# Optimization experiments

Hardware: AMD Instinct MI355X
Metric: run time of the kernel (lower is better)

## Reference

```python
import jax, jax.numpy as jnp
import numpy as np

N = 100000
E = 3200000
F_IN = 128
HID = 64
NUM_GRAPHS = 512
NUM_CLASSES = 2


def setup_inputs() -> dict:
    key = jax.random.key(0)
    ks = jax.random.split(key, 8)
    x = jax.random.normal(ks[0], (N, F_IN), dtype=jnp.float32)
    edge_index = jax.random.randint(ks[1], (2, E), 0, N, dtype=jnp.int64)
    batch = jnp.sort(jax.random.randint(ks[2], (N,), 0, NUM_GRAPHS, dtype=jnp.int64))
    # Glorot-style init for GCN weights, PyTorch default-style for fc
    W1 = jax.random.normal(ks[3], (F_IN, HID), dtype=jnp.float32) * (1.0 / np.sqrt(F_IN))
    b1 = jnp.zeros((HID,), dtype=jnp.float32)
    W2 = jax.random.normal(ks[4], (HID, HID), dtype=jnp.float32) * (1.0 / np.sqrt(HID))
    b2 = jnp.zeros((HID,), dtype=jnp.float32)
    Wfc = jax.random.normal(ks[5], (HID, NUM_CLASSES), dtype=jnp.float32) * (1.0 / np.sqrt(HID))
    bfc = jax.random.normal(ks[6], (NUM_CLASSES,), dtype=jnp.float32) * 0.01
    return {"x": x, "edge_index": edge_index, "batch": batch,
            "W1": W1, "b1": b1, "W2": W2, "b2": b2, "Wfc": Wfc, "bfc": bfc}


def _gcn_conv(x, row, col, deg_inv_sqrt, W, b):
    """PyG GCNConv: out[col] += d^{-1/2}[row] d^{-1/2}[col] * (x W)[row], self-loops included in row/col."""
    h = x @ W  # [N, out_dim]
    norm = deg_inv_sqrt[row] * deg_inv_sqrt[col]  # [E+N]
    msgs = h[row] * norm[:, None]  # gather + scale
    out = jax.ops.segment_sum(msgs, col, num_segments=N)  # scatter-add
    return out + b


def reference(x, edge_index, batch, W1, b1, W2, b2, Wfc, bfc):
    # add self-loops once (shared normalization for both layers)
    loop = jnp.arange(N, dtype=edge_index.dtype)
    row = jnp.concatenate([edge_index[0], loop])  # sources
    col = jnp.concatenate([edge_index[1], loop])  # targets
    deg = jax.ops.segment_sum(jnp.ones_like(col, dtype=x.dtype), col, num_segments=N)
    deg_inv_sqrt = jnp.where(deg > 0, jax.lax.rsqrt(deg), 0.0)

    h = jax.nn.relu(_gcn_conv(x, row, col, deg_inv_sqrt, W1, b1))
    h = jax.nn.relu(_gcn_conv(h, row, col, deg_inv_sqrt, W2, b2))

    # global_mean_pool over batch ids
    sums = jax.ops.segment_sum(h, batch, num_segments=NUM_GRAPHS)  # [G, HID]
    counts = jax.ops.segment_sum(jnp.ones((N,), dtype=h.dtype), batch, num_segments=NUM_GRAPHS)
    pooled = sums / jnp.maximum(counts, 1.0)[:, None]

    # dropout p=0.5 is identity in eval mode
    return pooled @ Wfc + bfc  # [G, NUM_CLASSES]
```

## Files before the change

### kernel.cpp

```cpp
#include <hip/hip_runtime.h>

#define N_NODES   100000
#define N_EDGES   3200000
#define F_INP     128
#define HID       64
#define N_GRAPHS  512
#define N_CLASSES 2
#define BSH       8
#define BSZ       256
#define NB        391
#define SCAT_BLOCKS 1024
#define CHUNK     (N_EDGES / SCAT_BLOCKS)
#define CAP2      8960

__device__ __forceinline__ unsigned short f2bf(float f) {
    unsigned int u = __float_as_uint(f);
    return (unsigned short)((u + 0x7FFFu + ((u >> 16) & 1u)) >> 16);
}
__device__ __forceinline__ float bf_lo(unsigned int u) { return __uint_as_float(u << 16); }
__device__ __forceinline__ float bf_hi(unsigned int u) { return __uint_as_float(u & 0xFFFF0000u); }

__global__ __launch_bounds__(256) void scatterX(const int* __restrict__ ei,
                                                int* __restrict__ gcur,
                                                int* __restrict__ pairs) {
    __shared__ int lcnt[NB];
    __shared__ int lbase[NB];
    __shared__ int lcur[NB];
    const int tid = threadIdx.x;
    for (int i = tid; i < NB; i += 256) { lcnt[i] = 0; lcur[i] = 0; }
    __syncthreads();
    const int e0 = blockIdx.x * CHUNK;
    for (int e = e0 + tid; e < e0 + CHUNK; e += 256)
        atomicAdd(&lcnt[ei[N_EDGES + e] >> BSH], 1);
    __syncthreads();
    for (int i = tid; i < NB; i += 256) {
        int c = lcnt[i];
        lbase[i] = c ? atomicAdd(&gcur[i], c) : 0;
    }
    __syncthreads();
    for (int e = e0 + tid; e < e0 + CHUNK; e += 256) {
        int c = ei[N_EDGES + e];
        int r = ei[e];
        int b = c >> BSH;
        int off = atomicAdd(&lcur[b], 1);
        int pos = lbase[b] + off;
        if (pos < CAP2)
            pairs[b * CAP2 + pos] = r | ((c & (BSZ - 1)) << 17);
    }
}

__global__ __launch_bounds__(512) void bscan_kernel(const int* __restrict__ gcur,
                                                    int* __restrict__ boff,
                                                    int* __restrict__ offs) {
    __shared__ int s[512];
    const int tid = threadIdx.x;
    const int v = (tid < NB) ? min(gcur[tid], CAP2) : 0;
    s[tid] = v;
    __syncthreads();
    for (int d = 1; d < 512; d <<= 1) {
        int t = (tid >= d) ? s[tid - d] : 0;
        __syncthreads();
        s[tid] += t;
        __syncthreads();
    }
    if (tid <= NB) boff[tid] = s[tid] - v;
    if (tid == NB) offs[N_NODES] = s[tid];
}

__global__ __launch_bounds__(512) void csrX(const int* __restrict__ pairs,
                                            const int* __restrict__ gcur,
                                            const int* __restrict__ boff,
                                            int* __restrict__ adj,
                                            int* __restrict__ offs,
                                            float* __restrict__ dis) {
    __shared__ int sedge[CAP2];
    __shared__ int cnt[BSZ];
    __shared__ int sc[BSZ];
    __shared__ int base[BSZ];
    __shared__ int cur[BSZ];
    const int tid = threadIdx.x;
    const int b = blockIdx.x;
    const int m = min(gcur[b], CAP2);
    const int dst = boff[b];
    if (tid < BSZ) { cnt[tid] = 0; cur[tid] = 0; }
    __syncthreads();
    for (int i = tid; i < m; i += 512) {
        int v = pairs[b * CAP2 + i];
        sedge[i] = v;
        atomicAdd(&cnt[v >> 17], 1);
    }
    __syncthreads();
    if (tid < BSZ) sc[tid] = cnt[tid];
    __syncthreads();
    for (int d = 1; d < BSZ; d <<= 1) {
        int t = (tid >= d && tid < BSZ) ? sc[tid - d] : 0;
        __syncthreads();
        if (tid < BSZ) sc[tid] += t;
        __syncthreads();
    }
    if (tid < BSZ) base[tid] = dst + sc[tid] - cnt[tid];
    __syncthreads();
    for (int i = tid; i < m; i += 512) {
        int v = sedge[i];
        int lc = v >> 17;
        int o = atomicAdd(&cur[lc], 1);
        adj[base[lc] + o] = v & 131071;
    }
    const int n = (b << BSH) + tid;
    if (tid < BSZ && n < N_NODES) {
        offs[n] = base[tid];
        dis[n] = rsqrtf((float)cnt[tid] + 1.0f);
    }
}

#define MM1_ROWS 32
#define XS_LD    132
__global__ __launch_bounds__(256) void mm1_kernel(const float* __restrict__ x,
                                                  const float* __restrict__ W1,
                                                  const float* __restrict__ dis,
                                                  unsigned short* __restrict__ p) {
    __shared__ float xs[MM1_ROWS * XS_LD];
    __shared__ float ws[F_INP * HID];
    for (int i = threadIdx.x; i < F_INP * HID / 4; i += 256)
        ((float4*)ws)[i] = ((const float4*)W1)[i];
    const int row_base = blockIdx.x * MM1_ROWS;
    for (int i = threadIdx.x; i < MM1_ROWS * (F_INP / 4); i += 256) {
        int r = i >> 5, c4 = i & 31;
        int gr = row_base + r;
        float4 v = make_float4(0.f, 0.f, 0.f, 0.f);
        if (gr < N_NODES) v = *(const float4*)(x + (size_t)gr * F_INP + c4 * 4);
        *(float4*)(xs + r * XS_LD + c4 * 4) = v;
    }
    __syncthreads();
    const int tx = threadIdx.x & 15;
    const int ty = threadIdx.x >> 4;
    float acc[2][4] = {};
#pragma unroll 4
    for (int k = 0; k < F_INP; k += 4) {
        float4 a0 = *(const float4*)(xs + ty * XS_LD + k);
        float4 a1 = *(const float4*)(xs + (ty + 16) * XS_LD + k);
        float4 w0 = *(const float4*)(ws + (k + 0) * HID + tx * 4);
        float4 w1 = *(const float4*)(ws + (k + 1) * HID + tx * 4);
        float4 w2 = *(const float4*)(ws + (k + 2) * HID + tx * 4);
        float4 w3 = *(const float4*)(ws + (k + 3) * HID + tx * 4);
        acc[0][0] += a0.x * w0.x + a0.y * w1.x + a0.z * w2.x + a0.w * w3.x;
        acc[0][1] += a0.x * w0.y + a0.y * w1.y + a0.z * w2.y + a0.w * w3.y;
        acc[0][2] += a0.x * w0.z + a0.y * w1.z + a0.z * w2.z + a0.w * w3.z;
        acc[0][3] += a0.x * w0.w + a0.y * w1.w + a0.z * w2.w + a0.w * w3.w;
        acc[1][0] += a1.x * w0.x + a1.y * w1.x + a1.z * w2.x + a1.w * w3.x;
        acc[1][1] += a1.x * w0.y + a1.y * w1.y + a1.z * w2.y + a1.w * w3.y;
        acc[1][2] += a1.x * w0.z + a1.y * w1.z + a1.z * w2.z + a1.w * w3.z;
        acc[1][3] += a1.x * w0.w + a1.y * w1.w + a1.z * w2.w + a1.w * w3.w;
    }
#pragma unroll
    for (int i = 0; i < 2; ++i) {
        int rr = row_base + ty + 16 * i;
        if (rr < N_NODES) {
            float d = dis[rr];
            ushort4 o;
            o.x = f2bf(d * acc[i][0]);
            o.y = f2bf(d * acc[i][1]);
            o.z = f2bf(d * acc[i][2]);
            o.w = f2bf(d * acc[i][3]);
            *(ushort4*)(p + (size_t)rr * HID + tx * 4) = o;
        }
    }
}

#define HS_LD 72
__global__ __launch_bounds__(256) void mm2_kernel(const unsigned short* __restrict__ hb,
                                                  const float* __restrict__ W2,
                                                  const float* __restrict__ dis,
                                                  unsigned short* __restrict__ p) {
    __shared__ unsigned short hs[64 * HS_LD];
    __shared__ float ws[HID * HID];
    for (int i = threadIdx.x; i < HID * HID / 4; i += 256)
        ((float4*)ws)[i] = ((const float4*)W2)[i];
    const int row_base = blockIdx.x * 64;
    for (int i = threadIdx.x; i < 64 * (HID / 8); i += 256) {
        int r = i >> 3, c8 = i & 7;
        int gr = row_base + r;
        uint4 v = make_uint4(0u, 0u, 0u, 0u);
        if (gr < N_NODES) v = *(const uint4*)(hb + (size_t)gr * HID + c8 * 8);
        *(uint4*)(hs + r * HS_LD + c8 * 8) = v;
    }
    __syncthreads();
    const int tx = threadIdx.x & 15;
    const int ty = threadIdx.x >> 4;
    float acc[4][4] = {};
#pragma unroll 2
    for (int k = 0; k < HID; k += 8) {
        uint4 a[4];
#pragma unroll
        for (int i = 0; i < 4; ++i)
            a[i] = *(const uint4*)(hs + (ty + 16 * i) * HS_LD + k);
        float4 w[8];
#pragma unroll
        for (int m = 0; m < 8; ++m)
            w[m] = *(const float4*)(ws + (k + m) * HID + tx * 4);
#pragma unroll
        for (int i = 0; i < 4; ++i) {
            float h0 = bf_lo(a[i].x), h1 = bf_hi(a[i].x);
            float h2 = bf_lo(a[i].y), h3 = bf_hi(a[i].y);
            float h4 = bf_lo(a[i].z), h5 = bf_hi(a[i].z);
            float h6 = bf_lo(a[i].w), h7 = bf_hi(a[i].w);
            acc[i][0] += h0 * w[0].x + h1 * w[1].x + h2 * w[2].x + h3 * w[3].x
                       + h4 * w[4].x + h5 * w[5].x + h6 * w[6].x + h7 * w[7].x;
            acc[i][1] += h0 * w[0].y + h1 * w[1].y + h2 * w[2].y + h3 * w[3].y
                       + h4 * w[4].y + h5 * w[5].y + h6 * w[6].y + h7 * w[7].y;
            acc[i][2] += h0 * w[0].z + h1 * w[1].z + h2 * w[2].z + h3 * w[3].z
                       + h4 * w[4].z + h5 * w[5].z + h6 * w[6].z + h7 * w[7].z;
            acc[i][3] += h0 * w[0].w + h1 * w[1].w + h2 * w[2].w + h3 * w[3].w
                       + h4 * w[4].w + h5 * w[5].w + h6 * w[6].w + h7 * w[7].w;
        }
    }
#pragma unroll
    for (int i = 0; i < 4; ++i) {
        int rr = row_base + ty + 16 * i;
        if (rr < N_NODES) {
            float d = dis[rr];
            ushort4 o;
            o.x = f2bf(d * acc[i][0]);
            o.y = f2bf(d * acc[i][1]);
            o.z = f2bf(d * acc[i][2]);
            o.w = f2bf(d * acc[i][3]);
            *(ushort4*)(p + (size_t)rr * HID + tx * 4) = o;
        }
    }
}

__device__ __forceinline__ float gather_node(const unsigned short* __restrict__ p,
                                             const int* __restrict__ adj,
                                             int c, int beg, int end, int q, int g) {
    float acc[8];
    {
        uint4 s = *(const uint4*)(p + (size_t)c * HID + g * 8);
        float sm = (q == 0) ? 1.f : 0.f;
        acc[0] = sm * bf_lo(s.x); acc[1] = sm * bf_hi(s.x);
        acc[2] = sm * bf_lo(s.y); acc[3] = sm * bf_hi(s.y);
        acc[4] = sm * bf_lo(s.z); acc[5] = sm * bf_hi(s.z);
        acc[6] = sm * bf_lo(s.w); acc[7] = sm * bf_hi(s.w);
    }
    int e = beg;
    for (; e + 32 <= end; e += 32) {
        int r0 = adj[e + q];
        int r1 = adj[e + 8 + q];
        int r2 = adj[e + 16 + q];
        int r3 = adj[e + 24 + q];
        uint4 v0 = *(const uint4*)(p + (size_t)r0 * HID + g * 8);
        uint4 v1 = *(const uint4*)(p + (size_t)r1 * HID + g * 8);
        uint4 v2 = *(const uint4*)(p + (size_t)r2 * HID + g * 8);
        uint4 v3 = *(const uint4*)(p + (size_t)r3 * HID + g * 8);
        acc[0] += (bf_lo(v0.x) + bf_lo(v1.x)) + (bf_lo(v2.x) + bf_lo(v3.x));
        acc[1] += (bf_hi(v0.x) + bf_hi(v1.x)) + (bf_hi(v2.x) + bf_hi(v3.x));
        acc[2] += (bf_lo(v0.y) + bf_lo(v1.y)) + (bf_lo(v2.y) + bf_lo(v3.y));
        acc[3] += (bf_hi(v0.y) + bf_hi(v1.y)) + (bf_hi(v2.y) + bf_hi(v3.y));
        acc[4] += (bf_lo(v0.z) + bf_lo(v1.z)) + (bf_lo(v2.z) + bf_lo(v3.z));
        acc[5] += (bf_hi(v0.z) + bf_hi(v1.z)) + (bf_hi(v2.z) + bf_hi(v3.z));
        acc[6] += (bf_lo(v0.w) + bf_lo(v1.w)) + (bf_lo(v2.w) + bf_lo(v3.w));
        acc[7] += (bf_hi(v0.w) + bf_hi(v1.w)) + (bf_hi(v2.w) + bf_hi(v3.w));
    }
    for (; e + 16 <= end; e += 16) {
        int r0 = adj[e + q];
        int r1 = adj[e + 8 + q];
        uint4 v0 = *(const uint4*)(p + (size_t)r0 * HID + g * 8);
        uint4 v1 = *(const uint4*)(p + (size_t)r1 * HID + g * 8);
        acc[0] += bf_lo(v0.x) + bf_lo(v1.x); acc[1] += bf_hi(v0.x) + bf_hi(v1.x);
        acc[2] += bf_lo(v0.y) + bf_lo(v1.y); acc[3] += bf_hi(v0.y) + bf_hi(v1.y);
        acc[4] += bf_lo(v0.z) + bf_lo(v1.z); acc[5] += bf_hi(v0.z) + bf_hi(v1.z);
        acc[6] += bf_lo(v0.w) + bf_lo(v1.w); acc[7] += bf_hi(v0.w) + bf_hi(v1.w);
    }
    for (; e < end; e += 8) {
        int idx = e + q;
        int r = adj[min(idx, end - 1)];
        float m = (idx < end) ? 1.f : 0.f;
        uint4 v = *(const uint4*)(p + (size_t)r * HID + g * 8);
        acc[0] = fmaf(m, bf_lo(v.x), acc[0]); acc[1] = fmaf(m, bf_hi(v.x), acc[1]);
        acc[2] = fmaf(m, bf_lo(v.y), acc[2]); acc[3] = fmaf(m, bf_hi(v.y), acc[3]);
        acc[4] = fmaf(m, bf_lo(v.z), acc[4]); acc[5] = fmaf(m, bf_hi(v.z), acc[5]);
        acc[6] = fmaf(m, bf_lo(v.w), acc[6]); acc[7] = fmaf(m, bf_hi(v.w), acc[7]);
    }
    const bool q0 = (q & 1) != 0, q1 = (q & 2) != 0, q2 = (q & 4) != 0;
    float b0 = (q0 ? acc[1] : acc[0]) + __shfl_xor(q0 ? acc[0] : acc[1], 8, 64);
    float b1 = (q0 ? acc[3] : acc[2]) + __shfl_xor(q0 ? acc[2] : acc[3], 8, 64);
    float b2 = (q0 ? acc[5] : acc[4]) + __shfl_xor(q0 ? acc[4] : acc[5], 8, 64);
    float b3 = (q0 ? acc[7] : acc[6]) + __shfl_xor(q0 ? acc[6] : acc[7], 8, 64);
    float c0 = (q1 ? b1 : b0) + __shfl_xor(q1 ? b0 : b1, 16, 64);
    float c1 = (q1 ? b3 : b2) + __shfl_xor(q1 ? b2 : b3, 16, 64);
    return (q2 ? c1 : c0) + __shfl_xor(q2 ? c0 : c1, 32, 64);
}

__global__ __launch_bounds__(256) void gather1_kernel(const unsigned short* __restrict__ p,
                                                      const int* __restrict__ adj,
                                                      const int* __restrict__ offs,
                                                      const float* __restrict__ dis,
                                                      const float* __restrict__ b1,
                                                      unsigned short* __restrict__ hb) {
    const int lane = threadIdx.x & 63;
    const int q = lane >> 3, g = lane & 7;
    const int gwave = (blockIdx.x * blockDim.x + threadIdx.x) >> 6;
    const int nwaves = (gridDim.x * blockDim.x) >> 6;
    const int per = (N_NODES + nwaves - 1) / nwaves;
    const int c0 = gwave * per;
    const int c1 = min(N_NODES, c0 + per);
    const float bj = b1[g * 8 + q];
    if (c0 >= c1) return;
    int beg = offs[c0];
    for (int c = c0; c < c1; ++c) {
        const int end = offs[c + 1];
        float val = gather_node(p, adj, c, beg, end, q, g);
        hb[(size_t)c * HID + g * 8 + q] = f2bf(fmaxf(dis[c] * val + bj, 0.f));
        beg = end;
    }
}

__global__ __launch_bounds__(256) void gather2_kernel(const unsigned short* __restrict__ p,
                                                      const int* __restrict__ adj,
                                                      const int* __restrict__ offs,
                                                      const float* __restrict__ dis,
                                                      const float* __restrict__ b2,
                                                      const int* __restrict__ batch,
                                                      float* __restrict__ sums) {
    const int lane = threadIdx.x & 63;
    const int q = lane >> 3, g = lane & 7;
    const int gwave = (blockIdx.x * blockDim.x + threadIdx.x) >> 6;
    const int nwaves = (gridDim.x * blockDim.x) >> 6;
    const int per = (N_NODES + nwaves - 1) / nwaves;
    const int c0 = gwave * per;
    const int c1 = min(N_NODES, c0 + per);
    const float bj = b2[g * 8 + q];
    const int feat = g * 8 + q;
    float part = 0.f;
    int gc = -1;
    if (c0 >= c1) return;
    int beg = offs[c0];
    for (int c = c0; c < c1; ++c) {
        const int end = offs[c + 1];
        float val = gather_node(p, adj, c, beg, end, q, g);
        float v = fmaxf(dis[c] * val + bj, 0.f);
        int gid = batch[c];
        if (gid != gc) {
            if (gc >= 0) atomicAdd(&sums[(size_t)gc * HID + feat], part);
            part = 0.f;
            gc = gid;
        }
        part += v;
        beg = end;
    }
    if (gc >= 0) atomicAdd(&sums[(size_t)gc * HID + feat], part);
}

__global__ void fc_kernel(const float* __restrict__ sums, const int* __restrict__ batch,
                          const float* __restrict__ Wfc, const float* __restrict__ bfc,
                          float* __restrict__ out) {
    const int g = blockIdx.x;
    const int j = threadIdx.x;
    int lo = 0, hi = N_NODES;
    while (lo < hi) { int m = (lo + hi) >> 1; if (batch[m] < g) lo = m + 1; else hi = m; }
    const int l0 = lo;
    lo = 0; hi = N_NODES;
    while (lo < hi) { int m = (lo + hi) >> 1; if (batch[m] < g + 1) lo = m + 1; else hi = m; }
    float cnt = fmaxf((float)(lo - l0), 1.0f);
    float pj = sums[(size_t)g * HID + j] / cnt;
    float a0 = pj * Wfc[j * N_CLASSES + 0];
    float a1 = pj * Wfc[j * N_CLASSES + 1];
    for (int off = 32; off > 0; off >>= 1) {
        a0 += __shfl_down(a0, off, 64);
        a1 += __shfl_down(a1, off, 64);
    }
    if (j == 0) {
        out[g * N_CLASSES + 0] = a0 + bfc[0];
        out[g * N_CLASSES + 1] = a1 + bfc[1];
    }
}

extern "C" void kernel_launch(void* const* d_in, const int* in_sizes, int n_in,
                              void* d_out, int out_size, void* d_ws, size_t ws_size,
                              hipStream_t stream) {
    const float* x     = (const float*)d_in[0];
    const int*   ei    = (const int*)d_in[1];
    const int*   batch = (const int*)d_in[2];
    const float* W1    = (const float*)d_in[3];
    const float* b1    = (const float*)d_in[4];
    const float* W2    = (const float*)d_in[5];
    const float* b2    = (const float*)d_in[6];
    const float* Wfc   = (const float*)d_in[7];
    const float* bfc   = (const float*)d_in[8];
    float* out = (float*)d_out;

    char* ws = (char*)d_ws;
    size_t off = 0;
    auto alloc = [&](size_t bytes) -> void* {
        void* pp = ws + off;
        off += (bytes + 255) & ~(size_t)255;
        return pp;
    };
    int*   gcur   = (int*)alloc((size_t)NB * 4);
    float* sums   = (float*)alloc((size_t)N_GRAPHS * HID * 4);
    int*   boff   = (int*)alloc((size_t)(NB + 1) * 4);
    int*   offs   = (int*)alloc((size_t)(N_NODES + 1) * 4);
    float* dis    = (float*)alloc((size_t)N_NODES * 4);
    int*   pairs  = (int*)alloc((size_t)NB * CAP2 * 4);
    int*   adj    = (int*)alloc((size_t)N_EDGES * 4);
    unsigned short* p  = (unsigned short*)alloc((size_t)N_NODES * HID * 2);
    unsigned short* hb = (unsigned short*)alloc((size_t)N_NODES * HID * 2);

    hipMemsetAsync(gcur, 0, (size_t)((char*)(sums + N_GRAPHS * HID) - (char*)gcur), stream);

    scatterX<<<SCAT_BLOCKS, 256, 0, stream>>>(ei, gcur, pairs);
    bscan_kernel<<<1, 512, 0, stream>>>(gcur, boff, offs);
    csrX<<<NB, 512, 0, stream>>>(pairs, gcur, boff, adj, offs, dis);
    mm1_kernel<<<(N_NODES + MM1_ROWS - 1) / MM1_ROWS, 256, 0, stream>>>(x, W1, dis, p);
    gather1_kernel<<<2048, 256, 0, stream>>>(p, adj, offs, dis, b1, hb);
    mm2_kernel<<<(N_NODES + 63) / 64, 256, 0, stream>>>(hb, W2, dis, p);
    gather2_kernel<<<2048, 256, 0, stream>>>(p, adj, offs, dis, b2, batch, sums);
    fc_kernel<<<N_GRAPHS, 64, 0, stream>>>(sums, batch, Wfc, bfc, out);
}
```

Before: 363.3 us.

## Fuse edge scatter with first matmul and fold block scan into CSR build

Measured after the change: 348.2 us. -4.2%, faster.

```diff
diff --git a/kernel.cpp b/kernel.cpp
--- a/kernel.cpp
+++ b/kernel.cpp
@@ -9,9 +9,12 @@
 #define BSH       8
 #define BSZ       256
 #define NB        391
-#define SCAT_BLOCKS 1024
+#define SCAT_BLOCKS 256
 #define CHUNK     (N_EDGES / SCAT_BLOCKS)
 #define CAP2      8960
+#define MM1_ROWS  32
+#define XS_LD     132
+#define MM1_BLOCKS ((N_NODES + MM1_ROWS - 1) / MM1_ROWS)
 
 __device__ __forceinline__ unsigned short f2bf(float f) {
     unsigned int u = __float_as_uint(f);
@@ -20,68 +23,109 @@
 __device__ __forceinline__ float bf_lo(unsigned int u) { return __uint_as_float(u << 16); }
 __device__ __forceinline__ float bf_hi(unsigned int u) { return __uint_as_float(u & 0xFFFF0000u); }
 
-__global__ __launch_bounds__(256) void scatterX(const int* __restrict__ ei,
-                                                int* __restrict__ gcur,
-                                                int* __restrict__ pairs) {
-    __shared__ int lcnt[NB];
-    __shared__ int lbase[NB];
-    __shared__ int lcur[NB];
+__global__ __launch_bounds__(256) void fused_pre(const int* __restrict__ ei,
+                                                 int* __restrict__ gcur,
+                                                 int* __restrict__ pairs,
+                                                 const float* __restrict__ x,
+                                                 const float* __restrict__ W1,
+                                                 float* __restrict__ praw) {
+    __shared__ __align__(16) char smem[(MM1_ROWS * XS_LD + F_INP * HID) * 4];
     const int tid = threadIdx.x;
-    for (int i = tid; i < NB; i += 256) { lcnt[i] = 0; lcur[i] = 0; }
-    __syncthreads();
-    const int e0 = blockIdx.x * CHUNK;
-    for (int e = e0 + tid; e < e0 + CHUNK; e += 256)
-        atomicAdd(&lcnt[ei[N_EDGES + e] >> BSH], 1);
-    __syncthreads();
-    for (int i = tid; i < NB; i += 256) {
-        int c = lcnt[i];
-        lbase[i] = c ? atomicAdd(&gcur[i], c) : 0;
-    }
-    __syncthreads();
-    for (int e = e0 + tid; e < e0 + CHUNK; e += 256) {
-        int c = ei[N_EDGES + e];
-        int r = ei[e];
-        int b = c >> BSH;
-        int off = atomicAdd(&lcur[b], 1);
-        int pos = lbase[b] + off;
-        if (pos < CAP2)
-            pairs[b * CAP2 + pos] = r | ((c & (BSZ - 1)) << 17);
-    }
-}
-
-__global__ __launch_bounds__(512) void bscan_kernel(const int* __restrict__ gcur,
-                                                    int* __restrict__ boff,
-                                                    int* __restrict__ offs) {
-    __shared__ int s[512];
-    const int tid = threadIdx.x;
-    const int v = (tid < NB) ? min(gcur[tid], CAP2) : 0;
-    s[tid] = v;
-    __syncthreads();
-    for (int d = 1; d < 512; d <<= 1) {
-        int t = (tid >= d) ? s[tid - d] : 0;
-        __syncthreads();
-        s[tid] += t;
-        __syncthreads();
-    }
-    if (tid <= NB) boff[tid] = s[tid] - v;
-    if (tid == NB) offs[N_NODES] = s[tid];
+    if (blockIdx.x < SCAT_BLOCKS) {
+        int* lcnt = (int*)smem;
+        int* lbase = lcnt + NB;
+        int* lcur = lbase + NB;
+        for (int i = tid; i < NB; i += 256) { lcnt[i] = 0; lcur[i] = 0; }
+        __syncthreads();
+        const int e0 = blockIdx.x * CHUNK;
+        for (int e = e0 + tid; e < e0 + CHUNK; e += 256)
+            atomicAdd(&lcnt[ei[N_EDGES + e] >> BSH], 1);
+        __syncthreads();
+        for (int i = tid; i < NB; i += 256) {
+            int c = lcnt[i];
+            lbase[i] = c ? atomicAdd(&gcur[i], c) : 0;
+        }
+        __syncthreads();
+        for (int e = e0 + tid; e < e0 + CHUNK; e += 256) {
+            int c = ei[N_EDGES + e];
+            int r = ei[e];
+            int b = c >> BSH;
+            int off = atomicAdd(&lcur[b], 1);
+            int pos = lbase[b] + off;
+            if (pos < CAP2)
+                pairs[b * CAP2 + pos] = r | ((c & (BSZ - 1)) << 17);
+        }
+    } else {
+        float* xs = (float*)smem;
+        float* ws = xs + MM1_ROWS * XS_LD;
+        for (int i = tid; i < F_INP * HID / 4; i += 256)
+            ((float4*)ws)[i] = ((const float4*)W1)[i];
+        const int row_base = (blockIdx.x - SCAT_BLOCKS) * MM1_ROWS;
+        for (int i = tid; i < MM1_ROWS * (F_INP / 4); i += 256) {
+            int r = i >> 5, c4 = i & 31;
+            int gr = row_base + r;
+            float4 v = make_float4(0.f, 0.f, 0.f, 0.f);
+            if (gr < N_NODES) v = *(const float4*)(x + (size_t)gr * F_INP + c4 * 4);
+            *(float4*)(xs + r * XS_LD + c4 * 4) = v;
+        }
+        __syncthreads();
+        const int tx = tid & 15;
+        const int ty = tid >> 4;
+        float acc[2][4] = {};
+#pragma unroll 4
+        for (int k = 0; k < F_INP; k += 4) {
+            float4 a0 = *(const float4*)(xs + ty * XS_LD + k);
+            float4 a1 = *(const float4*)(xs + (ty + 16) * XS_LD + k);
+            float4 w0 = *(const float4*)(ws + (k + 0) * HID + tx * 4);
+            float4 w1 = *(const float4*)(ws + (k + 1) * HID + tx * 4);
+            float4 w2 = *(const float4*)(ws + (k + 2) * HID + tx * 4);
+            float4 w3 = *(const float4*)(ws + (k + 3) * HID + tx * 4);
+            acc[0][0] += a0.x * w0.x + a0.y * w1.x + a0.z * w2.x + a0.w * w3.x;
+            acc[0][1] += a0.x * w0.y + a0.y * w1.y + a0.z * w2.y + a0.w * w3.y;
+            acc[0][2] += a0.x * w0.z + a0.y * w1.z + a0.z * w2.z + a0.w * w3.z;
+            acc[0][3] += a0.x * w0.w + a0.y * w1.w + a0.z * w2.w + a0.w * w3.w;
+            acc[1][0] += a1.x * w0.x + a1.y * w1.x + a1.z * w2.x + a1.w * w3.x;
+            acc[1][1] += a1.x * w0.y + a1.y * w1.y + a1.z * w2.y + a1.w * w3.y;
+            acc[1][2] += a1.x * w0.z + a1.y * w1.z + a1.z * w2.z + a1.w * w3.z;
+            acc[1][3] += a1.x * w0.w + a1.y * w1.w + a1.z * w2.w + a1.w * w3.w;
+        }
+#pragma unroll
+        for (int i = 0; i < 2; ++i) {
+            int rr = row_base + ty + 16 * i;
+            if (rr < N_NODES)
+                *(float4*)(praw + (size_t)rr * HID + tx * 4) =
+                    make_float4(acc[i][0], acc[i][1], acc[i][2], acc[i][3]);
+        }
+    }
 }
 
 __global__ __launch_bounds__(512) void csrX(const int* __restrict__ pairs,
                                             const int* __restrict__ gcur,
-                                            const int* __restrict__ boff,
+                                            const float* __restrict__ praw,
+                                            unsigned short* __restrict__ p,
                                             int* __restrict__ adj,
                                             int* __restrict__ offs,
                                             float* __restrict__ dis) {
     __shared__ int sedge[CAP2];
+    __shared__ int gs[512];
     __shared__ int cnt[BSZ];
     __shared__ int sc[BSZ];
     __shared__ int base[BSZ];
     __shared__ int cur[BSZ];
     const int tid = threadIdx.x;
     const int b = blockIdx.x;
-    const int m = min(gcur[b], CAP2);
-    const int dst = boff[b];
+    gs[tid] = (tid < NB) ? min(gcur[tid], CAP2) : 0;
+    __syncthreads();
+    for (int d = 1; d < 512; d <<= 1) {
+        int t = (tid >= d) ? gs[tid - d] : 0;
+        __syncthreads();
+        gs[tid] += t;
+        __syncthreads();
+    }
+    const int vb = min(gcur[b], CAP2);
+    const int dst = gs[b] - vb;
+    const int m = vb;
+    if (b == 0 && tid == 0) offs[N_NODES] = gs[511];
     if (tid < BSZ) { cnt[tid] = 0; cur[tid] = 0; }
     __syncthreads();
     for (int i = tid; i < m; i += 512) {
@@ -111,59 +155,14 @@
         offs[n] = base[tid];
         dis[n] = rsqrtf((float)cnt[tid] + 1.0f);
     }
-}
-
-#define MM1_ROWS 32
-#define XS_LD    132
-__global__ __launch_bounds__(256) void mm1_kernel(const float* __restrict__ x,
-                                                  const float* __restrict__ W1,
-                                                  const float* __restrict__ dis,
-                                                  unsigned short* __restrict__ p) {
-    __shared__ float xs[MM1_ROWS * XS_LD];
-    __shared__ float ws[F_INP * HID];
-    for (int i = threadIdx.x; i < F_INP * HID / 4; i += 256)
-        ((float4*)ws)[i] = ((const float4*)W1)[i];
-    const int row_base = blockIdx.x * MM1_ROWS;
-    for (int i = threadIdx.x; i < MM1_ROWS * (F_INP / 4); i += 256) {
-        int r = i >> 5, c4 = i & 31;
-        int gr = row_base + r;
-        float4 v = make_float4(0.f, 0.f, 0.f, 0.f);
-        if (gr < N_NODES) v = *(const float4*)(x + (size_t)gr * F_INP + c4 * 4);
-        *(float4*)(xs + r * XS_LD + c4 * 4) = v;
-    }
-    __syncthreads();
-    const int tx = threadIdx.x & 15;
-    const int ty = threadIdx.x >> 4;
-    float acc[2][4] = {};
-#pragma unroll 4
-    for (int k = 0; k < F_INP; k += 4) {
-        float4 a0 = *(const float4*)(xs + ty * XS_LD + k);
-        float4 a1 = *(const float4*)(xs + (ty + 16) * XS_LD + k);
-        float4 w0 = *(const float4*)(ws + (k + 0) * HID + tx * 4);
-        float4 w1 = *(const float4*)(ws + (k + 1) * HID + tx * 4);
-        float4 w2 = *(const float4*)(ws + (k + 2) * HID + tx * 4);
-        float4 w3 = *(const float4*)(ws + (k + 3) * HID + tx * 4);
-        acc[0][0] += a0.x * w0.x + a0.y * w1.x + a0.z * w2.x + a0.w * w3.x;
-        acc[0][1] += a0.x * w0.y + a0.y * w1.y + a0.z * w2.y + a0.w * w3.y;
-        acc[0][2] += a0.x * w0.z + a0.y * w1.z + a0.z * w2.z + a0.w * w3.z;
-        acc[0][3] += a0.x * w0.w + a0.y * w1.w + a0.z * w2.w + a0.w * w3.w;
-        acc[1][0] += a1.x * w0.x + a1.y * w1.x + a1.z * w2.x + a1.w * w3.x;
-        acc[1][1] += a1.x * w0.y + a1.y * w1.y + a1.z * w2.y + a1.w * w3.y;
-        acc[1][2] += a1.x * w0.z + a1.y * w1.z + a1.z * w2.z + a1.w * w3.z;
-        acc[1][3] += a1.x * w0.w + a1.y * w1.w + a1.z * w2.w + a1.w * w3.w;
-    }
-#pragma unroll
-    for (int i = 0; i < 2; ++i) {
-        int rr = row_base + ty + 16 * i;
-        if (rr < N_NODES) {
-            float d = dis[rr];
-            ushort4 o;
-            o.x = f2bf(d * acc[i][0]);
-            o.y = f2bf(d * acc[i][1]);
-            o.z = f2bf(d * acc[i][2]);
-            o.w = f2bf(d * acc[i][3]);
-            *(ushort4*)(p + (size_t)rr * HID + tx * 4) = o;
-        }
+    const int nrows = min(BSZ, N_NODES - (b << BSH));
+    const float2* pr = (const float2*)(praw + ((size_t)(b << BSH)) * HID);
+    unsigned int* p32 = (unsigned int*)(p + ((size_t)(b << BSH)) * HID);
+    for (int i = tid; i < nrows * 32; i += 512) {
+        int row = i >> 5;
+        float d = rsqrtf((float)cnt[row] + 1.0f);
+        float2 w = pr[i];
+        p32[i] = (unsigned int)f2bf(w.x * d) | ((unsigned int)f2bf(w.y * d) << 16);
     }
 }
 
@@ -397,20 +396,18 @@
     };
     int*   gcur   = (int*)alloc((size_t)NB * 4);
     float* sums   = (float*)alloc((size_t)N_GRAPHS * HID * 4);
-    int*   boff   = (int*)alloc((size_t)(NB + 1) * 4);
     int*   offs   = (int*)alloc((size_t)(N_NODES + 1) * 4);
     float* dis    = (float*)alloc((size_t)N_NODES * 4);
     int*   pairs  = (int*)alloc((size_t)NB * CAP2 * 4);
     int*   adj    = (int*)alloc((size_t)N_EDGES * 4);
+    float* praw   = (float*)alloc((size_t)N_NODES * HID * 4);
     unsigned short* p  = (unsigned short*)alloc((size_t)N_NODES * HID * 2);
     unsigned short* hb = (unsigned short*)alloc((size_t)N_NODES * HID * 2);
 
     hipMemsetAsync(gcur, 0, (size_t)((char*)(sums + N_GRAPHS * HID) - (char*)gcur), stream);
 
-    scatterX<<<SCAT_BLOCKS, 256, 0, stream>>>(ei, gcur, pairs);
-    bscan_kernel<<<1, 512, 0, stream>>>(gcur, boff, offs);
-    csrX<<<NB, 512, 0, stream>>>(pairs, gcur, boff, adj, offs, dis);
-    mm1_kernel<<<(N_NODES + MM1_ROWS - 1) / MM1_ROWS, 256, 0, stream>>>(x, W1, dis, p);
+    fused_pre<<<SCAT_BLOCKS + MM1_BLOCKS, 256, 0, stream>>>(ei, gcur, pairs, x, W1, praw);
+    csrX<<<NB, 512, 0, stream>>>(pairs, gcur, praw, p, adj, offs, dis);
     gather1_kernel<<<2048, 256, 0, stream>>>(p, adj, offs, dis, b1, hb);
     mm2_kernel<<<(N_NODES + 63) / 64, 256, 0, stream>>>(hb, W2, dis, p);
     gather2_kernel<<<2048, 256, 0, stream>>>(p, adj, offs, dis, b2, batch, sums);
```
